# Performance work log

Hardware: AMD Instinct MI355X
Metric: run time of the kernel (lower is better)

The kernel has to match this reference:

```python
import jax, jax.numpy as jnp
import numpy as np

B, N, DIM, H = 4, 128, 512, 8
EPS = 1e-5

def _lin(k, fan_in, fan_out):
    kw, kb = jax.random.split(k)
    w = jax.random.normal(kw, (fan_in, fan_out), jnp.float32) * 0.02
    b = jax.random.normal(kb, (fan_out,), jnp.float32) * 0.02
    return w, b

def setup_inputs() -> dict:
    key = jax.random.key(0)
    ks = jax.random.split(key, 12)
    node_features = jax.random.normal(ks[0], (B, N, DIM), jnp.float32)
    edge_features = jax.random.normal(ks[1], (B, N, N, DIM), jnp.float32)
    adjacency_weights = jax.random.uniform(ks[2], (B, N, N), jnp.float32)
    Wn_w, Wn_b = _lin(ks[3], DIM, DIM)
    We1_w, We1_b = _lin(ks[4], 3 * DIM, DIM)
    We2_w, We2_b = _lin(ks[5], DIM, H)
    Wm_w, Wm_b = _lin(ks[6], DIM, DIM)
    Wu1_w, Wu1_b = _lin(ks[7], 3 * DIM, DIM)
    Wu2_w, Wu2_b = _lin(ks[8], DIM, DIM)
    Wo_w, Wo_b = _lin(ks[9], DIM, DIM)
    ln_g = jnp.ones((DIM,), jnp.float32)
    ln_b = jnp.zeros((DIM,), jnp.float32)
    return dict(node_features=node_features, edge_features=edge_features,
                adjacency_weights=adjacency_weights,
                Wn_w=Wn_w, Wn_b=Wn_b, We1_w=We1_w, We1_b=We1_b,
                We2_w=We2_w, We2_b=We2_b, Wm_w=Wm_w, Wm_b=Wm_b,
                Wu1_w=Wu1_w, Wu1_b=Wu1_b, Wu2_w=Wu2_w, Wu2_b=Wu2_b,
                Wo_w=Wo_w, Wo_b=Wo_b, ln_g=ln_g, ln_b=ln_b)

def _layernorm(x, g, b):
    mu = jnp.mean(x, axis=-1, keepdims=True)
    var = jnp.var(x, axis=-1, keepdims=True)
    return (x - mu) * jax.lax.rsqrt(var + EPS) * g + b

def reference(node_features, edge_features, adjacency_weights,
              Wn_w, Wn_b, We1_w, We1_b, We2_w, We2_b, Wm_w, Wm_b,
              Wu1_w, Wu1_b, Wu2_w, Wu2_b, Wo_w, Wo_b, ln_g, ln_b):
    b, n, d = node_features.shape
    h = node_features @ Wn_w + Wn_b                       # (B,N,D)
    h_i = jnp.broadcast_to(h[:, :, None, :], (b, n, n, d))
    h_j = jnp.broadcast_to(h[:, None, :, :], (b, n, n, d))
    edge_input = jnp.concatenate([h_i, h_j, edge_features], axis=-1)  # (B,N,N,3D)
    # edge attention MLP
    e = jax.nn.leaky_relu(edge_input @ We1_w + We1_b, negative_slope=0.2)
    attn = e @ We2_w + We2_b                              # (B,N,N,H)
    attn = jax.nn.softmax(attn, axis=2)                   # softmax over j
    attn = attn * adjacency_weights[..., None]
    # messages: W_msg applied to h_j == W_msg(h) broadcast; aggregate with mean attn
    messages = h @ Wm_w + Wm_b                            # (B,N,D)
    attn_mean = jnp.mean(attn, axis=-1)                   # (B,N,N)
    aggregated = jnp.einsum('bij,bjd->bid', attn_mean, messages)
    updated_nodes = _layernorm(node_features + (aggregated @ Wo_w + Wo_b), ln_g, ln_b)
    # edge update MLP (exact GELU as in torch default)
    u = jax.nn.gelu(edge_input @ Wu1_w + Wu1_b, approximate=False)
    updated_edges = edge_features + (u @ Wu2_w + Wu2_b)
    return updated_nodes, updated_edges
```

## Files before the change

kernel.cpp:

```cpp
#include <hip/hip_runtime.h>
#include <hip/hip_bf16.h>


typedef __bf16  bf16x8 __attribute__((ext_vector_type(8)));
typedef float   f32x4  __attribute__((ext_vector_type(4)));
typedef __hip_bfloat16 bfloat;

#define AS1 __attribute__((address_space(1)))
#define AS3 __attribute__((address_space(3)))

__device__ __forceinline__ void g2l16(const void* g, void* l) {
  __builtin_amdgcn_global_load_lds((AS1 void*)g, (AS3 void*)l, 16, 0, 0);
}

__device__ __forceinline__ float ldf(const void* p, size_t i, int f) {
  return f ? ((const float*)p)[i] : __bfloat162float(((const bfloat*)p)[i]);
}
__device__ __forceinline__ void stf(void* p, size_t i, float v, int f) {
  if (f) ((float*)p)[i] = v;
  else   ((bfloat*)p)[i] = __float2bfloat16(v);
}

__device__ __forceinline__ float gelu_f(float x) {
  float y = 0.7978845608028654f * (x + 0.044715f * x * x * x);
  float e = __expf(2.0f * y);
  float t = 1.0f - 2.0f / (e + 1.0f);
  return 0.5f * x * (1.0f + t);
}

__global__ __launch_bounds__(256) void detect_dtype(const unsigned short* nu, int* flag) {
  __shared__ int bad;
  if (threadIdx.x == 0) bad = 0;
  __syncthreads();
  int local = 0;
  for (int i = threadIdx.x; i < 4096; i += 256) {
    int ex = (nu[i] >> 7) & 0xFF;
    if (ex >= 0xC0) local = 1;
  }
  if (local) atomicOr(&bad, 1);
  __syncthreads();
  if (threadIdx.x == 0) *flag = bad;
}

__global__ __launch_bounds__(256) void cvt_edge(const float* E, const int* flag, void* dout) {
  if (*flag == 0) return;
  const int e = blockIdx.x & 7;
  const int x = blockIdx.x >> 3;
  const int m = x >> 5;
  const int h = (x >> 4) & 1;
  const int s = x & 15;
  const int c = 2 * e + 16 * m + h;
  const int t = threadIdx.x;
  const int rloc = s * 4 + (t >> 6);
  const int c8 = t & 63;
  const float* src = E + ((size_t)c * 64 + rloc) * 512 + (size_t)c8 * 8;
  f32x4 lo = *(const f32x4*)src;
  f32x4 hi = *(const f32x4*)(src + 4);
  bf16x8 v;
  v[0] = (__bf16)lo[0]; v[1] = (__bf16)lo[1]; v[2] = (__bf16)lo[2]; v[3] = (__bf16)lo[3];
  v[4] = (__bf16)hi[0]; v[5] = (__bf16)hi[1]; v[6] = (__bf16)hi[2]; v[7] = (__bf16)hi[3];
  char* eb = (char*)dout + 1048576;
  *(bf16x8*)(eb + (size_t)c * 131072 + (size_t)rloc * 1024 + (size_t)c8 * 16) = v;
}

__global__ __launch_bounds__(256) void transpose3(const void* We1, const void* Wu1,
                                                  const void* Wu2, const int* flag,
                                                  bfloat* WtA, bfloat* WtB, bfloat* WtC) {
  const int f = *flag;
  int idx = blockIdx.x * 256 + threadIdx.x;
  int m = idx >> 18;
  int r = idx & 262143;
  int n = r >> 9, k = r & 511;
  size_t si = (size_t)k * 512 + n;
  float v;
  bfloat* dst;
  if (m == 0)      { v = ldf(We1, 524288 + si, f); dst = WtA; }
  else if (m == 1) { v = ldf(Wu1, 524288 + si, f); dst = WtB; }
  else             { v = ldf(Wu2, si, f);          dst = WtC; }
  dst[(size_t)n * 512 + k] = __float2bfloat16(v);
}

__global__ __launch_bounds__(256) void small_gemm(const void* A, int amode, const void* W,
                                                  size_t woff, const void* bias,
                                                  const int* flag, float* out) {
  const int f = *flag;
  const int af = amode ? 1 : f;
  __shared__ float sA[4][512];
  const int t = threadIdx.x;
  const int r0 = blockIdx.x * 4;
  for (int idx = t; idx < 2048; idx += 256)
    sA[idx >> 9][idx & 511] = ldf(A, (size_t)(r0 + (idx >> 9)) * 512 + (idx & 511), af);
  __syncthreads();
  float acc0[4] = {0.f, 0.f, 0.f, 0.f}, acc1[4] = {0.f, 0.f, 0.f, 0.f};
#pragma unroll 4
  for (int k = 0; k < 512; ++k) {
    float w0 = ldf(W, woff + (size_t)k * 512 + t, f);
    float w1 = ldf(W, woff + (size_t)k * 512 + t + 256, f);
#pragma unroll
    for (int r = 0; r < 4; ++r) {
      acc0[r] += sA[r][k] * w0;
      acc1[r] += sA[r][k] * w1;
    }
  }
  float b0 = bias ? ldf(bias, t, f) : 0.f;
  float b1 = bias ? ldf(bias, t + 256, f) : 0.f;
#pragma unroll
  for (int r = 0; r < 4; ++r) {
    out[(size_t)(r0 + r) * 512 + t] = acc0[r] + b0;
    out[(size_t)(r0 + r) * 512 + t + 256] = acc1[r] + b1;
  }
}

__global__ __launch_bounds__(256) void fused5(const float* h, const void* We1, const void* We1b,
                                              const void* Wu1, const void* Wu1b, const void* Wm,
                                              const void* Wmb, const int* flag, float* P1,
                                              float* Q1, float* P2, float* Q2, float* msgv) {
  const int f = *flag;
  const void* W;
  size_t woff = 0;
  const void* bias = nullptr;
  float* out;
  switch (blockIdx.y) {
    case 0:  W = We1; bias = We1b; out = P1; break;
    case 1:  W = We1; woff = 262144; out = Q1; break;
    case 2:  W = Wu1; bias = Wu1b; out = P2; break;
    case 3:  W = Wu1; woff = 262144; out = Q2; break;
    default: W = Wm;  bias = Wmb;  out = msgv; break;
  }
  __shared__ float sA[4][512];
  const int t = threadIdx.x;
  const int r0 = blockIdx.x * 4;
  for (int idx = t; idx < 2048; idx += 256)
    sA[idx >> 9][idx & 511] = h[(size_t)(r0 + (idx >> 9)) * 512 + (idx & 511)];
  __syncthreads();
  float acc0[4] = {0.f, 0.f, 0.f, 0.f}, acc1[4] = {0.f, 0.f, 0.f, 0.f};
#pragma unroll 4
  for (int k = 0; k < 512; ++k) {
    float w0 = ldf(W, woff + (size_t)k * 512 + t, f);
    float w1 = ldf(W, woff + (size_t)k * 512 + t + 256, f);
#pragma unroll
    for (int r = 0; r < 4; ++r) {
      acc0[r] += sA[r][k] * w0;
      acc1[r] += sA[r][k] * w1;
    }
  }
  float b0 = bias ? ldf(bias, t, f) : 0.f;
  float b1 = bias ? ldf(bias, t + 256, f) : 0.f;
#pragma unroll
  for (int r = 0; r < 4; ++r) {
    out[(size_t)(r0 + r) * 512 + t] = acc0[r] + b0;
    out[(size_t)(r0 + r) * 512 + t + 256] = acc1[r] + b1;
  }
}

__global__ __launch_bounds__(256) void k3_edge_mlp(const void* E, const bfloat* WtA,
                                                   const bfloat* WtB, const float* P1,
                                                   const float* Q1, const float* P2,
                                                   const float* Q2, const void* We2,
                                                   const int* flag, float* logits4, void* dout) {
  const int f = *flag;
  __shared__ __align__(16) char smem[53248];
  f32x4 acc[4][4];
#pragma unroll
  for (int mi = 0; mi < 4; ++mi)
#pragma unroll
    for (int ni = 0; ni < 4; ++ni) acc[mi][ni] = (f32x4){0.f, 0.f, 0.f, 0.f};

  const int idx0 = blockIdx.x;
  const int bm = (idx0 >> 6) * 8 + (idx0 & 7);
  const int bn = (idx0 >> 3) & 7;
  const bool attn = bn < 4;
  const bfloat* Bg = attn ? WtA + (size_t)bn * 65536 : WtB + (size_t)(bn - 4) * 65536;
  const bfloat* Eb = (const bfloat*)E;
  const char* eb = (const char*)dout + 1048576;

  const int t = threadIdx.x;
  const int lane = t & 63;
  const int wave = t >> 6;
  const int wrow = wave >> 1, wcol = wave & 1;
  const int l15 = lane & 15;
  const int q = lane >> 4;
  const int blockcol = (attn ? bn : (bn - 4)) * 128;

  const int row0 = t >> 2, p0 = t & 3, g0 = p0 ^ ((row0 >> 1) & 3);
  const int row1 = 64 + row0, g1 = p0 ^ ((row1 >> 1) & 3);
  const char* srcB0 = (const char*)Bg + ((size_t)row0 * 512 + g0 * 8) * 2;
  const char* srcB1 = (const char*)Bg + ((size_t)row1 * 512 + g1 * 8) * 2;
  const char* srcA0;
  const char* srcA1;
  const int gr0 = bm * 128 + row0, gr1 = gr0 + 64;
  if (f) {
    srcA0 = eb + (size_t)(gr0 >> 6) * 131072 + (size_t)(gr0 & 63) * 1024 + (size_t)g0 * 16;
    srcA1 = eb + (size_t)(gr1 >> 6) * 131072 + (size_t)(gr1 & 63) * 1024 + (size_t)g1 * 16;
  } else {
    srcA0 = (const char*)Eb + ((size_t)gr0 * 512 + g0 * 8) * 2;
    srcA1 = (const char*)Eb + ((size_t)gr1 * 512 + g1 * 8) * 2;
  }
  const int dst0 = wave * 1024;
  const int dst1 = 4096 + wave * 1024;

  auto stage = [&](int kt2, int sel2) {
    char* dA = smem + sel2 * 8192;
    char* dB = smem + 24576 + sel2 * 8192;
    const int koff = kt2 * 64;
    g2l16(srcA0 + koff, dA + dst0);
    g2l16(srcA1 + koff, dA + dst1);
    g2l16(srcB0 + koff, dB + dst0);
    g2l16(srcB1 + koff, dB + dst1);
  };

  stage(0, 0);
  stage(1, 1);

  if (attn) {
    for (int idx = t; idx < 2048; idx += 256) {
      const int n = idx >> 7, k = idx & 127;
      float v = (n < 8) ? ldf(We2, (size_t)(blockcol + k) * 8 + n, f) : 0.f;
      *(bfloat*)(smem + 49152 + (size_t)n * 256 + (((k >> 3) ^ n) * 16) + (k & 7) * 2) =
          __float2bfloat16(v);
    }
  }

  const int fA = (wrow * 64 + l15) * 64 + ((q ^ ((l15 >> 1) & 3)) * 16);
  const int fB = (wcol * 64 + l15) * 64 + ((q ^ ((l15 >> 1) & 3)) * 16);

#pragma unroll
  for (int kt = 0; kt < 16; ++kt) {
    if (kt < 15) asm volatile("s_waitcnt vmcnt(4)" ::: "memory");
    else         asm volatile("s_waitcnt vmcnt(0)" ::: "memory");
    __builtin_amdgcn_s_barrier();
    if (kt < 14) stage(kt + 2, (kt + 2) % 3);
    const char* A = smem + (kt % 3) * 8192;
    const char* B = smem + 24576 + (kt % 3) * 8192;
    bf16x8 afr[4], bfr[4];
#pragma unroll
    for (int mi = 0; mi < 4; ++mi) afr[mi] = *(const bf16x8*)(A + fA + mi * 1024);
#pragma unroll
    for (int ni = 0; ni < 4; ++ni) bfr[ni] = *(const bf16x8*)(B + fB + ni * 1024);
#pragma unroll
    for (int mi = 0; mi < 4; ++mi)
#pragma unroll
      for (int ni = 0; ni < 4; ++ni)
        acc[mi][ni] =
            __builtin_amdgcn_mfma_f32_16x16x32_bf16(afr[mi], bfr[ni], acc[mi][ni], 0, 0, 0);
  }

  const int b = bm >> 7;
  const float* P = attn ? P1 : P2;
  const float* Qm = attn ? Q1 : Q2;
  float pv[4];
#pragma unroll
  for (int ni = 0; ni < 4; ++ni)
    pv[ni] = P[(size_t)bm * 512 + blockcol + wcol * 64 + ni * 16 + l15];

  __syncthreads();

  if (!attn) {
#pragma unroll
    for (int mi = 0; mi < 4; ++mi)
#pragma unroll
      for (int rr = 0; rr < 4; ++rr) {
        const int j = wrow * 64 + mi * 16 + q * 4 + rr;
#pragma unroll
        for (int ni = 0; ni < 4; ++ni) {
          const int cc = wcol * 64 + ni * 16 + l15;
          const int c = blockcol + cc;
          float x = acc[mi][ni][rr] + pv[ni] + Qm[((size_t)b * 128 + j) * 512 + c];
          *(bfloat*)(smem + (size_t)j * 256 + (((cc >> 3) ^ (j & 15)) * 16) + (cc & 7) * 2) =
              __float2bfloat16(gelu_f(x));
        }
      }
    __syncthreads();
    char* ubase = (char*)dout + (f ? (1048576 + 65536) : 524288);
    const size_t blkstride = f ? 131072 : 65536;
#pragma unroll
    for (int rd = 0; rd < 8; ++rd) {
      const int j = rd * 16 + (t >> 4);
      const int ch = t & 15;
      f32x4 v = *(const f32x4*)(smem + (size_t)j * 256 + ((ch ^ (j & 15)) * 16));
      const size_t m = (size_t)bm * 128 + j;
      *(f32x4*)(ubase + (m >> 6) * blkstride + (m & 63) * 1024 + (size_t)blockcol * 2 +
                (size_t)ch * 16) = v;
    }
  } else {
#pragma unroll
    for (int mi = 0; mi < 4; ++mi)
#pragma unroll
      for (int rr = 0; rr < 4; ++rr) {
        const int j = wrow * 64 + mi * 16 + q * 4 + rr;
#pragma unroll
        for (int ni = 0; ni < 4; ++ni) {
          const int cc = wcol * 64 + ni * 16 + l15;
          const int c = blockcol + cc;
          float x = acc[mi][ni][rr] + pv[ni] + Qm[((size_t)b * 128 + j) * 512 + c];
          float e4 = (x >= 0.f) ? x : 0.2f * x;
          *(bfloat*)(smem + (size_t)j * 256 + (((cc >> 3) ^ (j & 15)) * 16) + (cc & 7) * 2) =
              __float2bfloat16(e4);
        }
      }
    __syncthreads();
    f32x4 acc2[2];
    acc2[0] = (f32x4){0.f, 0.f, 0.f, 0.f};
    acc2[1] = (f32x4){0.f, 0.f, 0.f, 0.f};
    const int jb = wave * 32;
#pragma unroll
    for (int ks = 0; ks < 4; ++ks) {
      const int gA = ((ks * 4 + q) ^ l15) * 16;
      bf16x8 a0 = *(const bf16x8*)(smem + (size_t)(jb + l15) * 256 + gA);
      bf16x8 a1 = *(const bf16x8*)(smem + (size_t)(jb + 16 + l15) * 256 + gA);
      bf16x8 bb = *(const bf16x8*)(smem + 49152 + (size_t)l15 * 256 + gA);
      acc2[0] = __builtin_amdgcn_mfma_f32_16x16x32_bf16(a0, bb, acc2[0], 0, 0, 0);
      acc2[1] = __builtin_amdgcn_mfma_f32_16x16x32_bf16(a1, bb, acc2[1], 0, 0, 0);
    }
#pragma unroll
    for (int mi2 = 0; mi2 < 2; ++mi2)
#pragma unroll
      for (int rr = 0; rr < 4; ++rr) {
        if (l15 < 8) {
          const int j = jb + mi2 * 16 + q * 4 + rr;
          logits4[(((size_t)bn * 512 + bm) * 128 + j) * 8 + l15] = acc2[mi2][rr];
        }
      }
  }
}

__global__ __launch_bounds__(512) void k6_edge_out(const bfloat* WtC, const void* Wu2b,
                                                   const void* E, const int* flag, void* dout) {
  const int f = *flag;
  __shared__ __align__(16) char smem[110592];
  f32x4 acc[2][8];
#pragma unroll
  for (int mi = 0; mi < 2; ++mi)
#pragma unroll
    for (int ni = 0; ni < 8; ++ni) acc[mi][ni] = (f32x4){0.f, 0.f, 0.f, 0.f};

  const int e = blockIdx.x & 7;
  const int x = blockIdx.x >> 3;
  const int bm = 2 * e + 16 * (x >> 1) + (x & 1);
  const int t = threadIdx.x;
  const int lane = t & 63;
  const int wave = t >> 6;
  const int wm = wave >> 2, wn = wave & 3;
  const int l15 = lane & 15;
  const int q = lane >> 4;
  const size_t r0 = (size_t)bm * 64;
  const char* ua = (const char*)dout +
                   (f ? (1048576 + (size_t)bm * 131072 + 65536) : (524288 + (size_t)bm * 65536));

  const int iA = t & 255;
  const int rowA = iA >> 2, pA = iA & 3, gA = pA ^ ((rowA >> 1) & 3);
  const char* srcA = ua + (size_t)rowA * 1024 + (size_t)gA * 16;
  const int dstA = (wave & 3) * 1024;
  const char* srcB[4];
  int dstB[4];
#pragma unroll
  for (int c = 0; c < 4; ++c) {
    const int idx = c * 512 + t;
    const int row = idx >> 2, p = idx & 3, g = p ^ ((row >> 1) & 3);
    srcB[c] = (const char*)WtC + ((size_t)row * 512 + g * 8) * 2;
    dstB[c] = (c * 512 + wave * 64) * 16;
  }

  auto stage = [&](int kt2, int sel2) {
    const int koff = kt2 * 64;
    char* dA = smem + sel2 * 4096;
    char* dB = smem + 12288 + sel2 * 32768;
    g2l16(srcA + koff, dA + dstA);
#pragma unroll
    for (int c = 0; c < 4; ++c) g2l16(srcB[c] + koff, dB + dstB[c]);
  };

  stage(0, 0);
  stage(1, 1);

  const int swz = (q ^ ((l15 >> 1) & 3)) * 16;
  const int fAo = (wm * 32 + l15) * 64 + swz;
  const int fBo = (wn * 128 + l15) * 64 + swz;

#pragma unroll
  for (int kt = 0; kt < 16; ++kt) {
    if (kt < 15) asm volatile("s_waitcnt vmcnt(5)" ::: "memory");
    else         asm volatile("s_waitcnt vmcnt(0)" ::: "memory");
    __builtin_amdgcn_s_barrier();
    if (kt < 14) stage(kt + 2, (kt + 2) % 3);
    const char* sA = smem + (kt % 3) * 4096;
    const char* sB = smem + 12288 + (kt % 3) * 32768;
    bf16x8 afr[2], bfr[8];
#pragma unroll
    for (int mi = 0; mi < 2; ++mi) afr[mi] = *(const bf16x8*)(sA + fAo + mi * 1024);
#pragma unroll
    for (int ni = 0; ni < 8; ++ni) bfr[ni] = *(const bf16x8*)(sB + fBo + ni * 1024);
#pragma unroll
    for (int mi = 0; mi < 2; ++mi)
#pragma unroll
      for (int ni = 0; ni < 8; ++ni)
        acc[mi][ni] = __builtin_amdgcn_mfma_f32_16x16x32_bf16(afr[mi], bfr[ni], acc[mi][ni], 0, 0, 0);
  }
  float wb[8];
#pragma unroll
  for (int ni = 0; ni < 8; ++ni) wb[ni] = ldf(Wu2b, wn * 128 + ni * 16 + l15, f);
  const bfloat* eres = (const bfloat*)((const char*)dout + 1048576 + (size_t)bm * 131072);
#pragma unroll
  for (int mi = 0; mi < 2; ++mi)
#pragma unroll
    for (int rr = 0; rr < 4; ++rr) {
      const int j = wm * 32 + mi * 16 + q * 4 + rr;
#pragma unroll
      for (int ni = 0; ni < 8; ++ni) {
        const int c = wn * 128 + ni * 16 + l15;
        float r = f ? __bfloat162float(eres[(size_t)j * 512 + c])
                    : __bfloat162float(((const bfloat*)E)[(r0 + j) * 512 + c]);
        acc[mi][ni][rr] += wb[ni] + r;
      }
    }
  __syncthreads();
#pragma unroll
  for (int mi = 0; mi < 2; ++mi)
#pragma unroll
    for (int rr = 0; rr < 4; ++rr) {
      const int j = wm * 32 + mi * 16 + q * 4 + rr;
      const size_t row = r0 + j;
#pragma unroll
      for (int ni = 0; ni < 8; ++ni) {
        const int c = wn * 128 + ni * 16 + l15;
        stf(dout, 262144 + row * 512 + c, acc[mi][ni][rr], f);
      }
    }
}

__global__ __launch_bounds__(128) void softmax_mean(const float* logits4, const void* adj,
                                                    const int* flag, float* amean) {
  const int f = *flag;
  const int bi = blockIdx.x;
  const int j = threadIdx.x;
  const int wv = j >> 6;
  __shared__ float sred[2][8];
  f32x4 v0 = (f32x4){0.f, 0.f, 0.f, 0.f}, v1 = (f32x4){0.f, 0.f, 0.f, 0.f};
#pragma unroll
  for (int s = 0; s < 4; ++s) {
    const float* p = logits4 + (((size_t)s * 512 + bi) * 128 + j) * 8;
    v0 += *(const f32x4*)p;
    v1 += *(const f32x4*)(p + 4);
  }
  float xv[8], m[8];
#pragma unroll
  for (int k = 0; k < 4; ++k) { xv[k] = v0[k]; xv[4 + k] = v1[k]; }
#pragma unroll
  for (int h = 0; h < 8; ++h) m[h] = xv[h];
#pragma unroll
  for (int o = 1; o < 64; o <<= 1)
#pragma unroll
    for (int h = 0; h < 8; ++h) m[h] = fmaxf(m[h], __shfl_xor(m[h], o));
  if ((j & 63) == 0) {
#pragma unroll
    for (int h = 0; h < 8; ++h) sred[wv][h] = m[h];
  }
  __syncthreads();
  float ex[8], s8[8];
#pragma unroll
  for (int h = 0; h < 8; ++h) {
    float mx = fmaxf(sred[0][h], sred[1][h]);
    ex[h] = __expf(xv[h] - mx);
    s8[h] = ex[h];
  }
#pragma unroll
  for (int o = 1; o < 64; o <<= 1)
#pragma unroll
    for (int h = 0; h < 8; ++h) s8[h] += __shfl_xor(s8[h], o);
  __syncthreads();
  if ((j & 63) == 0) {
#pragma unroll
    for (int h = 0; h < 8; ++h) sred[wv][h] = s8[h];
  }
  __syncthreads();
  float macc = 0.f;
#pragma unroll
  for (int h = 0; h < 8; ++h) macc += ex[h] / (sred[0][h] + sred[1][h]);
  amean[(size_t)bi * 128 + j] = macc * 0.125f * ldf(adj, (size_t)bi * 128 + j, f);
}

__global__ __launch_bounds__(256) void node_fused(const float* amean, const float* msg,
                                                  const void* Wo, const void* Wob,
                                                  const void* node, const void* lng,
                                                  const void* lnb, const int* flag, void* dout) {
  const int f = *flag;
  const int bi = blockIdx.x;
  const int b = bi >> 7;
  const int t = threadIdx.x;
  __shared__ float am[128];
  __shared__ float sAgg[512];
  __shared__ float red[256];
  if (t < 128) am[t] = amean[(size_t)bi * 128 + t];
  __syncthreads();
  float a0 = 0.f, a1 = 0.f;
#pragma unroll 4
  for (int jj = 0; jj < 128; ++jj) {
    const float* mr = msg + ((size_t)b * 128 + jj) * 512;
    a0 += am[jj] * mr[t];
    a1 += am[jj] * mr[t + 256];
  }
  sAgg[t] = a0;
  sAgg[t + 256] = a1;
  __syncthreads();
  float v0 = 0.f, v1 = 0.f;
#pragma unroll 4
  for (int k = 0; k < 512; ++k) {
    float a = sAgg[k];
    v0 += a * ldf(Wo, (size_t)k * 512 + t, f);
    v1 += a * ldf(Wo, (size_t)k * 512 + t + 256, f);
  }
  v0 += ldf(Wob, t, f) + ldf(node, (size_t)bi * 512 + t, f);
  v1 += ldf(Wob, t + 256, f) + ldf(node, (size_t)bi * 512 + t + 256, f);
  red[t] = v0 + v1;
  __syncthreads();
  for (int s = 128; s > 0; s >>= 1) {
    if (t < s) red[t] += red[t + s];
    __syncthreads();
  }
  float mean = red[0] * (1.f / 512.f);
  __syncthreads();
  red[t] = (v0 - mean) * (v0 - mean) + (v1 - mean) * (v1 - mean);
  __syncthreads();
  for (int s = 128; s > 0; s >>= 1) {
    if (t < s) red[t] += red[t + s];
    __syncthreads();
  }
  float var = red[0] * (1.f / 512.f);
  float inv = rsqrtf(var + 1e-5f);
  stf(dout, (size_t)bi * 512 + t, (v0 - mean) * inv * ldf(lng, t, f) + ldf(lnb, t, f), f);
  stf(dout, (size_t)bi * 512 + t + 256,
      (v1 - mean) * inv * ldf(lng, t + 256, f) + ldf(lnb, t + 256, f), f);
}

extern "C" void kernel_launch(void* const* d_in, const int* in_sizes, int n_in, void* d_out,
                              int out_size, void* d_ws, size_t ws_size, hipStream_t stream) {
  (void)in_sizes; (void)n_in; (void)out_size; (void)ws_size;
  const void* node = d_in[0];
  const void* edge = d_in[1];
  const void* adj = d_in[2];
  const void* Wn_w = d_in[3];
  const void* Wn_b = d_in[4];
  const void* We1_w = d_in[5];
  const void* We1_b = d_in[6];
  const void* We2_w = d_in[7];
  const void* Wm_w = d_in[9];
  const void* Wm_b = d_in[10];
  const void* Wu1_w = d_in[11];
  const void* Wu1_b = d_in[12];
  const void* Wu2_w = d_in[13];
  const void* Wu2_b = d_in[14];
  const void* Wo_w = d_in[15];
  const void* Wo_b = d_in[16];
  const void* ln_g = d_in[17];
  const void* ln_b = d_in[18];

  char* w = (char*)d_ws;
  int* flag = (int*)w;        w += 256;
  float* h = (float*)w;       w += 262144 * 4;
  float* P1 = (float*)w;      w += 262144 * 4;
  float* Q1 = (float*)w;      w += 262144 * 4;
  float* P2 = (float*)w;      w += 262144 * 4;
  float* Q2 = (float*)w;      w += 262144 * 4;
  float* msg = (float*)w;     w += 262144 * 4;
  float* logits4 = (float*)w; w += (size_t)4 * 524288 * 4;
  float* amean = (float*)w;   w += 65536 * 4;
  bfloat* WtA = (bfloat*)w;   w += 262144 * 2;
  bfloat* WtB = (bfloat*)w;   w += 262144 * 2;
  bfloat* WtC = (bfloat*)w;   w += 262144 * 2;

  detect_dtype<<<1, 256, 0, stream>>>((const unsigned short*)node, flag);
  cvt_edge<<<16384, 256, 0, stream>>>((const float*)edge, flag, d_out);
  transpose3<<<3072, 256, 0, stream>>>(We1_w, Wu1_w, Wu2_w, flag, WtA, WtB, WtC);
  small_gemm<<<128, 256, 0, stream>>>(node, 0, Wn_w, 0, Wn_b, flag, h);
  fused5<<<dim3(128, 5), 256, 0, stream>>>(h, We1_w, We1_b, Wu1_w, Wu1_b, Wm_w, Wm_b, flag,
                                           P1, Q1, P2, Q2, msg);
  k3_edge_mlp<<<4096, 256, 0, stream>>>(edge, WtA, WtB, P1, Q1, P2, Q2, We2_w, flag,
                                        logits4, d_out);
  softmax_mean<<<512, 128, 0, stream>>>(logits4, adj, flag, amean);
  node_fused<<<512, 256, 0, stream>>>(amean, msg, Wo_w, Wo_b, node, ln_g, ln_b, flag, d_out);
  k6_edge_out<<<1024, 512, 0, stream>>>(WtC, Wu2_b, edge, flag, d_out);
}
```

Baseline: 732.8 us.

## Use MFMA for node projections, fuse edge MLP column halves, batch node rows

The five per-node projections (P1, Q1, P2, Q2, msg) move from a scalar FP32 kernel to a bf16 MFMA tiled GEMM, using weights pre-transposed into bf16 by an extended transpose kernel and a bf16 copy of h. The edge MLP kernel now computes the attention and update column tiles in the same block, so each edge-feature A tile is loaded once for both products. This halves the grid and increases LDS and register use. The node update kernel handles four rows per block with wave-shuffle LayerNorm reductions, so each Wo and msg load is reused across four rows, and the projections now round to bf16 precision.

New measurement: 823.6 us. +12.4%, slower.

```diff
diff --git a/kernel.cpp b/kernel.cpp
--- a/kernel.cpp
+++ b/kernel.cpp
@@ -64,8 +64,11 @@
 }
 
 __global__ __launch_bounds__(256) void transpose3(const void* We1, const void* Wu1,
-                                                  const void* Wu2, const int* flag,
-                                                  bfloat* WtA, bfloat* WtB, bfloat* WtC) {
+                                                  const void* Wu2, const void* Wm,
+                                                  const int* flag,
+                                                  bfloat* WtA, bfloat* WtB, bfloat* WtC,
+                                                  bfloat* WtD, bfloat* WtE, bfloat* WtF,
+                                                  bfloat* WtG, bfloat* WtH) {
   const int f = *flag;
   int idx = blockIdx.x * 256 + threadIdx.x;
   int m = idx >> 18;
@@ -74,15 +77,22 @@
   size_t si = (size_t)k * 512 + n;
   float v;
   bfloat* dst;
-  if (m == 0)      { v = ldf(We1, 524288 + si, f); dst = WtA; }
-  else if (m == 1) { v = ldf(Wu1, 524288 + si, f); dst = WtB; }
-  else             { v = ldf(Wu2, si, f);          dst = WtC; }
+  switch (m) {
+    case 0:  v = ldf(We1, 524288 + si, f); dst = WtA; break;
+    case 1:  v = ldf(Wu1, 524288 + si, f); dst = WtB; break;
+    case 2:  v = ldf(Wu2, si, f);          dst = WtC; break;
+    case 3:  v = ldf(We1, si, f);          dst = WtD; break;
+    case 4:  v = ldf(We1, 262144 + si, f); dst = WtE; break;
+    case 5:  v = ldf(Wu1, si, f);          dst = WtF; break;
+    case 6:  v = ldf(Wu1, 262144 + si, f); dst = WtG; break;
+    default: v = ldf(Wm, si, f);           dst = WtH; break;
+  }
   dst[(size_t)n * 512 + k] = __float2bfloat16(v);
 }
 
 __global__ __launch_bounds__(256) void small_gemm(const void* A, int amode, const void* W,
                                                   size_t woff, const void* bias,
-                                                  const int* flag, float* out) {
+                                                  const int* flag, float* out, bfloat* outb) {
   const int f = *flag;
   const int af = amode ? 1 : f;
   __shared__ float sA[4][512];
@@ -106,51 +116,110 @@
   float b1 = bias ? ldf(bias, t + 256, f) : 0.f;
 #pragma unroll
   for (int r = 0; r < 4; ++r) {
-    out[(size_t)(r0 + r) * 512 + t] = acc0[r] + b0;
-    out[(size_t)(r0 + r) * 512 + t + 256] = acc1[r] + b1;
-  }
-}
-
-__global__ __launch_bounds__(256) void fused5(const float* h, const void* We1, const void* We1b,
-                                              const void* Wu1, const void* Wu1b, const void* Wm,
-                                              const void* Wmb, const int* flag, float* P1,
-                                              float* Q1, float* P2, float* Q2, float* msgv) {
-  const int f = *flag;
-  const void* W;
-  size_t woff = 0;
+    float o0 = acc0[r] + b0, o1 = acc1[r] + b1;
+    out[(size_t)(r0 + r) * 512 + t] = o0;
+    out[(size_t)(r0 + r) * 512 + t + 256] = o1;
+    if (outb) {
+      outb[(size_t)(r0 + r) * 512 + t] = __float2bfloat16(o0);
+      outb[(size_t)(r0 + r) * 512 + t + 256] = __float2bfloat16(o1);
+    }
+  }
+}
+
+__global__ __launch_bounds__(256) void fused5_mfma(const bfloat* hb, const bfloat* WtD,
+                                                   const bfloat* WtE, const bfloat* WtF,
+                                                   const bfloat* WtG, const bfloat* WtH,
+                                                   const void* We1b, const void* Wu1b,
+                                                   const void* Wmb, const int* flag,
+                                                   float* P1, float* Q1, float* P2, float* Q2,
+                                                   float* msgv) {
+  const int fl = *flag;
+  __shared__ __align__(16) char smem[49152];
+  f32x4 acc[4][4];
+#pragma unroll
+  for (int mi = 0; mi < 4; ++mi)
+#pragma unroll
+    for (int ni = 0; ni < 4; ++ni) acc[mi][ni] = (f32x4){0.f, 0.f, 0.f, 0.f};
+
+  const int bid = blockIdx.x;
+  const int g = bid >> 4, rb = (bid >> 2) & 3, cbv = bid & 3;
+  const bfloat* Wt;
   const void* bias = nullptr;
   float* out;
-  switch (blockIdx.y) {
-    case 0:  W = We1; bias = We1b; out = P1; break;
-    case 1:  W = We1; woff = 262144; out = Q1; break;
-    case 2:  W = Wu1; bias = Wu1b; out = P2; break;
-    case 3:  W = Wu1; woff = 262144; out = Q2; break;
-    default: W = Wm;  bias = Wmb;  out = msgv; break;
-  }
-  __shared__ float sA[4][512];
-  const int t = threadIdx.x;
-  const int r0 = blockIdx.x * 4;
-  for (int idx = t; idx < 2048; idx += 256)
-    sA[idx >> 9][idx & 511] = h[(size_t)(r0 + (idx >> 9)) * 512 + (idx & 511)];
-  __syncthreads();
-  float acc0[4] = {0.f, 0.f, 0.f, 0.f}, acc1[4] = {0.f, 0.f, 0.f, 0.f};
-#pragma unroll 4
-  for (int k = 0; k < 512; ++k) {
-    float w0 = ldf(W, woff + (size_t)k * 512 + t, f);
-    float w1 = ldf(W, woff + (size_t)k * 512 + t + 256, f);
-#pragma unroll
-    for (int r = 0; r < 4; ++r) {
-      acc0[r] += sA[r][k] * w0;
-      acc1[r] += sA[r][k] * w1;
-    }
-  }
-  float b0 = bias ? ldf(bias, t, f) : 0.f;
-  float b1 = bias ? ldf(bias, t + 256, f) : 0.f;
-#pragma unroll
-  for (int r = 0; r < 4; ++r) {
-    out[(size_t)(r0 + r) * 512 + t] = acc0[r] + b0;
-    out[(size_t)(r0 + r) * 512 + t + 256] = acc1[r] + b1;
-  }
+  switch (g) {
+    case 0:  Wt = WtD; bias = We1b; out = P1; break;
+    case 1:  Wt = WtE; out = Q1; break;
+    case 2:  Wt = WtF; bias = Wu1b; out = P2; break;
+    case 3:  Wt = WtG; out = Q2; break;
+    default: Wt = WtH; bias = Wmb; out = msgv; break;
+  }
+  const bfloat* Ag = hb + (size_t)rb * 65536;
+  const bfloat* Bg = Wt + (size_t)cbv * 65536;
+
+  const int t = threadIdx.x, lane = t & 63, wave = t >> 6;
+  const int wrow = wave >> 1, wcol = wave & 1;
+  const int l15 = lane & 15, q = lane >> 4;
+
+  const int row0 = t >> 2, p0 = t & 3, g0 = p0 ^ ((row0 >> 1) & 3);
+  const int row1 = 64 + row0, g1 = p0 ^ ((row1 >> 1) & 3);
+  const char* srcA0 = (const char*)(Ag + (size_t)row0 * 512 + g0 * 8);
+  const char* srcA1 = (const char*)(Ag + (size_t)row1 * 512 + g1 * 8);
+  const char* srcB0 = (const char*)(Bg + (size_t)row0 * 512 + g0 * 8);
+  const char* srcB1 = (const char*)(Bg + (size_t)row1 * 512 + g1 * 8);
+  const int dst0 = wave * 1024, dst1 = 4096 + wave * 1024;
+
+  auto stage = [&](int kt2, int sel2) {
+    const int koff = kt2 * 64;
+    char* dA = smem + sel2 * 8192;
+    char* dB = smem + 24576 + sel2 * 8192;
+    g2l16(srcA0 + koff, dA + dst0);
+    g2l16(srcA1 + koff, dA + dst1);
+    g2l16(srcB0 + koff, dB + dst0);
+    g2l16(srcB1 + koff, dB + dst1);
+  };
+  stage(0, 0);
+  stage(1, 1);
+
+  const int swz = (q ^ ((l15 >> 1) & 3)) * 16;
+  const int fA = (wrow * 64 + l15) * 64 + swz;
+  const int fB = (wcol * 64 + l15) * 64 + swz;
+
+#pragma unroll
+  for (int kt = 0; kt < 16; ++kt) {
+    if (kt < 15) asm volatile("s_waitcnt vmcnt(4)" ::: "memory");
+    else         asm volatile("s_waitcnt vmcnt(0)" ::: "memory");
+    __builtin_amdgcn_s_barrier();
+    if (kt < 14) stage(kt + 2, (kt + 2) % 3);
+    const char* A = smem + (kt % 3) * 8192;
+    const char* B = smem + 24576 + (kt % 3) * 8192;
+    bf16x8 afr[4], bfr[4];
+#pragma unroll
+    for (int mi = 0; mi < 4; ++mi) afr[mi] = *(const bf16x8*)(A + fA + mi * 1024);
+#pragma unroll
+    for (int ni = 0; ni < 4; ++ni) bfr[ni] = *(const bf16x8*)(B + fB + ni * 1024);
+#pragma unroll
+    for (int mi = 0; mi < 4; ++mi)
+#pragma unroll
+      for (int ni = 0; ni < 4; ++ni)
+        acc[mi][ni] =
+            __builtin_amdgcn_mfma_f32_16x16x32_bf16(afr[mi], bfr[ni], acc[mi][ni], 0, 0, 0);
+  }
+
+  float bv[4];
+#pragma unroll
+  for (int ni = 0; ni < 4; ++ni)
+    bv[ni] = bias ? ldf(bias, (size_t)cbv * 128 + wcol * 64 + ni * 16 + l15, fl) : 0.f;
+#pragma unroll
+  for (int mi = 0; mi < 4; ++mi)
+#pragma unroll
+    for (int rr = 0; rr < 4; ++rr) {
+      const int j = wrow * 64 + mi * 16 + q * 4 + rr;
+#pragma unroll
+      for (int ni = 0; ni < 4; ++ni) {
+        const int cc = wcol * 64 + ni * 16 + l15;
+        out[(size_t)(rb * 128 + j) * 512 + cbv * 128 + cc] = acc[mi][ni][rr] + bv[ni];
+      }
+    }
 }
 
 __global__ __launch_bounds__(256) void k3_edge_mlp(const void* E, const bfloat* WtA,
@@ -159,33 +228,38 @@
                                                    const float* Q2, const void* We2,
                                                    const int* flag, float* logits4, void* dout) {
   const int f = *flag;
-  __shared__ __align__(16) char smem[53248];
-  f32x4 acc[4][4];
+  __shared__ __align__(16) char smem[77824];
+  f32x4 accA[4][4], accU[4][4];
 #pragma unroll
   for (int mi = 0; mi < 4; ++mi)
 #pragma unroll
-    for (int ni = 0; ni < 4; ++ni) acc[mi][ni] = (f32x4){0.f, 0.f, 0.f, 0.f};
+    for (int ni = 0; ni < 4; ++ni) {
+      accA[mi][ni] = (f32x4){0.f, 0.f, 0.f, 0.f};
+      accU[mi][ni] = (f32x4){0.f, 0.f, 0.f, 0.f};
+    }
 
   const int idx0 = blockIdx.x;
-  const int bm = (idx0 >> 6) * 8 + (idx0 & 7);
-  const int bn = (idx0 >> 3) & 7;
-  const bool attn = bn < 4;
-  const bfloat* Bg = attn ? WtA + (size_t)bn * 65536 : WtB + (size_t)(bn - 4) * 65536;
+  const int bm = (idx0 >> 5) * 8 + (idx0 & 7);
+  const int cb = (idx0 >> 3) & 3;
+  const int blockcol = cb * 128;
+  const bfloat* BgA = WtA + (size_t)cb * 65536;
+  const bfloat* BgU = WtB + (size_t)cb * 65536;
   const bfloat* Eb = (const bfloat*)E;
   const char* eb = (const char*)dout + 1048576;
 
-  const int t = threadIdx.x;
-  const int lane = t & 63;
-  const int wave = t >> 6;
+  const int t = threadIdx.x, lane = t & 63, wave = t >> 6;
   const int wrow = wave >> 1, wcol = wave & 1;
-  const int l15 = lane & 15;
-  const int q = lane >> 4;
-  const int blockcol = (attn ? bn : (bn - 4)) * 128;
+  const int l15 = lane & 15, q = lane >> 4;
+
+  for (int idx = t; idx < 2048; idx += 256) {
+    const int n = idx >> 7, k = idx & 127;
+    float v = (n < 8) ? ldf(We2, (size_t)(blockcol + k) * 8 + n, f) : 0.f;
+    *(bfloat*)(smem + 73728 + (size_t)n * 256 + (((k >> 3) ^ n) * 16) + (k & 7) * 2) =
+        __float2bfloat16(v);
+  }
 
   const int row0 = t >> 2, p0 = t & 3, g0 = p0 ^ ((row0 >> 1) & 3);
   const int row1 = 64 + row0, g1 = p0 ^ ((row1 >> 1) & 3);
-  const char* srcB0 = (const char*)Bg + ((size_t)row0 * 512 + g0 * 8) * 2;
-  const char* srcB1 = (const char*)Bg + ((size_t)row1 * 512 + g1 * 8) * 2;
   const char* srcA0;
   const char* srcA1;
   const int gr0 = bm * 128 + row0, gr1 = gr0 + 64;
@@ -196,81 +270,91 @@
     srcA0 = (const char*)Eb + ((size_t)gr0 * 512 + g0 * 8) * 2;
     srcA1 = (const char*)Eb + ((size_t)gr1 * 512 + g1 * 8) * 2;
   }
-  const int dst0 = wave * 1024;
-  const int dst1 = 4096 + wave * 1024;
+  const int dstA0 = wave * 1024, dstA1 = 4096 + wave * 1024;
+
+  const char* srcB[4];
+  int dstB[4];
+#pragma unroll
+  for (int c = 0; c < 4; ++c) {
+    const int idx = c * 256 + t;
+    const int row = idx >> 2, p = idx & 3, gg = p ^ ((row >> 1) & 3);
+    const bfloat* base =
+        (row < 128) ? (BgA + (size_t)row * 512) : (BgU + (size_t)(row - 128) * 512);
+    srcB[c] = (const char*)base + gg * 16;
+    dstB[c] = (c * 256 + wave * 64) * 16;
+  }
 
   auto stage = [&](int kt2, int sel2) {
+    const int koff = kt2 * 64;
     char* dA = smem + sel2 * 8192;
-    char* dB = smem + 24576 + sel2 * 8192;
-    const int koff = kt2 * 64;
-    g2l16(srcA0 + koff, dA + dst0);
-    g2l16(srcA1 + koff, dA + dst1);
-    g2l16(srcB0 + koff, dB + dst0);
-    g2l16(srcB1 + koff, dB + dst1);
+    char* dB = smem + 24576 + sel2 * 16384;
+    g2l16(srcA0 + koff, dA + dstA0);
+    g2l16(srcA1 + koff, dA + dstA1);
+#pragma unroll
+    for (int c = 0; c < 4; ++c) g2l16(srcB[c] + koff, dB + dstB[c]);
   };
-
   stage(0, 0);
   stage(1, 1);
 
-  if (attn) {
-    for (int idx = t; idx < 2048; idx += 256) {
-      const int n = idx >> 7, k = idx & 127;
-      float v = (n < 8) ? ldf(We2, (size_t)(blockcol + k) * 8 + n, f) : 0.f;
-      *(bfloat*)(smem + 49152 + (size_t)n * 256 + (((k >> 3) ^ n) * 16) + (k & 7) * 2) =
-          __float2bfloat16(v);
-    }
-  }
-
-  const int fA = (wrow * 64 + l15) * 64 + ((q ^ ((l15 >> 1) & 3)) * 16);
-  const int fB = (wcol * 64 + l15) * 64 + ((q ^ ((l15 >> 1) & 3)) * 16);
+  const int swz = (q ^ ((l15 >> 1) & 3)) * 16;
+  const int fA = (wrow * 64 + l15) * 64 + swz;
+  const int fB = (wcol * 64 + l15) * 64 + swz;
 
 #pragma unroll
   for (int kt = 0; kt < 16; ++kt) {
-    if (kt < 15) asm volatile("s_waitcnt vmcnt(4)" ::: "memory");
+    if (kt < 15) asm volatile("s_waitcnt vmcnt(6)" ::: "memory");
     else         asm volatile("s_waitcnt vmcnt(0)" ::: "memory");
     __builtin_amdgcn_s_barrier();
     if (kt < 14) stage(kt + 2, (kt + 2) % 3);
     const char* A = smem + (kt % 3) * 8192;
-    const char* B = smem + 24576 + (kt % 3) * 8192;
-    bf16x8 afr[4], bfr[4];
+    const char* B = smem + 24576 + (kt % 3) * 16384;
+    bf16x8 afr[4], bfrA[4], bfrU[4];
 #pragma unroll
     for (int mi = 0; mi < 4; ++mi) afr[mi] = *(const bf16x8*)(A + fA + mi * 1024);
 #pragma unroll
-    for (int ni = 0; ni < 4; ++ni) bfr[ni] = *(const bf16x8*)(B + fB + ni * 1024);
+    for (int ni = 0; ni < 4; ++ni) bfrA[ni] = *(const bf16x8*)(B + fB + ni * 1024);
 #pragma unroll
     for (int mi = 0; mi < 4; ++mi)
 #pragma unroll
       for (int ni = 0; ni < 4; ++ni)
-        acc[mi][ni] =
-            __builtin_amdgcn_mfma_f32_16x16x32_bf16(afr[mi], bfr[ni], acc[mi][ni], 0, 0, 0);
+        accA[mi][ni] =
+            __builtin_amdgcn_mfma_f32_16x16x32_bf16(afr[mi], bfrA[ni], accA[mi][ni], 0, 0, 0);
+#pragma unroll
+    for (int ni = 0; ni < 4; ++ni) bfrU[ni] = *(const bf16x8*)(B + 8192 + fB + ni * 1024);
+#pragma unroll
+    for (int mi = 0; mi < 4; ++mi)
+#pragma unroll
+      for (int ni = 0; ni < 4; ++ni)
+        accU[mi][ni] =
+            __builtin_amdgcn_mfma_f32_16x16x32_bf16(afr[mi], bfrU[ni], accU[mi][ni], 0, 0, 0);
   }
 
   const int b = bm >> 7;
-  const float* P = attn ? P1 : P2;
-  const float* Qm = attn ? Q1 : Q2;
-  float pv[4];
-#pragma unroll
-  for (int ni = 0; ni < 4; ++ni)
-    pv[ni] = P[(size_t)bm * 512 + blockcol + wcol * 64 + ni * 16 + l15];
-
-  __syncthreads();
-
-  if (!attn) {
-#pragma unroll
-    for (int mi = 0; mi < 4; ++mi)
-#pragma unroll
-      for (int rr = 0; rr < 4; ++rr) {
-        const int j = wrow * 64 + mi * 16 + q * 4 + rr;
-#pragma unroll
-        for (int ni = 0; ni < 4; ++ni) {
-          const int cc = wcol * 64 + ni * 16 + l15;
-          const int c = blockcol + cc;
-          float x = acc[mi][ni][rr] + pv[ni] + Qm[((size_t)b * 128 + j) * 512 + c];
-          *(bfloat*)(smem + (size_t)j * 256 + (((cc >> 3) ^ (j & 15)) * 16) + (cc & 7) * 2) =
-              __float2bfloat16(gelu_f(x));
-        }
+  float pv1[4], pv2[4];
+#pragma unroll
+  for (int ni = 0; ni < 4; ++ni) {
+    const size_t o = (size_t)bm * 512 + blockcol + wcol * 64 + ni * 16 + l15;
+    pv1[ni] = P1[o];
+    pv2[ni] = P2[o];
+  }
+  __syncthreads();
+
+#pragma unroll
+  for (int mi = 0; mi < 4; ++mi)
+#pragma unroll
+    for (int rr = 0; rr < 4; ++rr) {
+      const int j = wrow * 64 + mi * 16 + q * 4 + rr;
+#pragma unroll
+      for (int ni = 0; ni < 4; ++ni) {
+        const int cc = wcol * 64 + ni * 16 + l15;
+        const int c = blockcol + cc;
+        float x = accU[mi][ni][rr] + pv2[ni] + Q2[((size_t)b * 128 + j) * 512 + c];
+        *(bfloat*)(smem + (size_t)j * 256 + (((cc >> 3) ^ (j & 15)) * 16) + (cc & 7) * 2) =
+            __float2bfloat16(gelu_f(x));
       }
-    __syncthreads();
+    }
+  __syncthreads();
+  {
     char* ubase = (char*)dout + (f ? (1048576 + 65536) : 524288);
     const size_t blkstride = f ? 131072 : 65536;
 #pragma unroll
@@ -282,23 +366,26 @@
       *(f32x4*)(ubase + (m >> 6) * blkstride + (m & 63) * 1024 + (size_t)blockcol * 2 +
                 (size_t)ch * 16) = v;
     }
-  } else {
-#pragma unroll
-    for (int mi = 0; mi < 4; ++mi)
-#pragma unroll
-      for (int rr = 0; rr < 4; ++rr) {
-        const int j = wrow * 64 + mi * 16 + q * 4 + rr;
-#pragma unroll
-        for (int ni = 0; ni < 4; ++ni) {
-          const int cc = wcol * 64 + ni * 16 + l15;
-          const int c = blockcol + cc;
-          float x = acc[mi][ni][rr] + pv[ni] + Qm[((size_t)b * 128 + j) * 512 + c];
-          float e4 = (x >= 0.f) ? x : 0.2f * x;
-          *(bfloat*)(smem + (size_t)j * 256 + (((cc >> 3) ^ (j & 15)) * 16) + (cc & 7) * 2) =
-              __float2bfloat16(e4);
-        }
+  }
+  __syncthreads();
+
+#pragma unroll
+  for (int mi = 0; mi < 4; ++mi)
+#pragma unroll
+    for (int rr = 0; rr < 4; ++rr) {
+      const int j = wrow * 64 + mi * 16 + q * 4 + rr;
+#pragma unroll
+      for (int ni = 0; ni < 4; ++ni) {
+        const int cc = wcol * 64 + ni * 16 + l15;
+        const int c = blockcol + cc;
+        float x = accA[mi][ni][rr] + pv1[ni] + Q1[((size_t)b * 128 + j) * 512 + c];
+        float e4 = (x >= 0.f) ? x : 0.2f * x;
+        *(bfloat*)(smem + (size_t)j * 256 + (((cc >> 3) ^ (j & 15)) * 16) + (cc & 7) * 2) =
+            __float2bfloat16(e4);
       }
-    __syncthreads();
+    }
+  __syncthreads();
+  {
     f32x4 acc2[2];
     acc2[0] = (f32x4){0.f, 0.f, 0.f, 0.f};
     acc2[1] = (f32x4){0.f, 0.f, 0.f, 0.f};
@@ -308,7 +395,7 @@
       const int gA = ((ks * 4 + q) ^ l15) * 16;
       bf16x8 a0 = *(const bf16x8*)(smem + (size_t)(jb + l15) * 256 + gA);
       bf16x8 a1 = *(const bf16x8*)(smem + (size_t)(jb + 16 + l15) * 256 + gA);
-      bf16x8 bb = *(const bf16x8*)(smem + 49152 + (size_t)l15 * 256 + gA);
+      bf16x8 bb = *(const bf16x8*)(smem + 73728 + (size_t)l15 * 256 + gA);
       acc2[0] = __builtin_amdgcn_mfma_f32_16x16x32_bf16(a0, bb, acc2[0], 0, 0, 0);
       acc2[1] = __builtin_amdgcn_mfma_f32_16x16x32_bf16(a1, bb, acc2[1], 0, 0, 0);
     }
@@ -318,7 +405,7 @@
       for (int rr = 0; rr < 4; ++rr) {
         if (l15 < 8) {
           const int j = jb + mi2 * 16 + q * 4 + rr;
-          logits4[(((size_t)bn * 512 + bm) * 128 + j) * 8 + l15] = acc2[mi2][rr];
+          logits4[(((size_t)cb * 512 + bm) * 128 + j) * 8 + l15] = acc2[mi2][rr];
         }
       }
   }
@@ -484,52 +571,95 @@
                                                   const void* node, const void* lng,
                                                   const void* lnb, const int* flag, void* dout) {
   const int f = *flag;
-  const int bi = blockIdx.x;
-  const int b = bi >> 7;
+  const int r0 = blockIdx.x * 4;
+  const int b = r0 >> 7;
   const int t = threadIdx.x;
-  __shared__ float am[128];
-  __shared__ float sAgg[512];
-  __shared__ float red[256];
-  if (t < 128) am[t] = amean[(size_t)bi * 128 + t];
-  __syncthreads();
-  float a0 = 0.f, a1 = 0.f;
-#pragma unroll 4
+  const int lane = t & 63, wave = t >> 6;
+  __shared__ float am[512];
+  __shared__ float sAgg[4][512];
+  __shared__ float sw[4][4];
+  __shared__ float sw2[4][4];
+  am[t] = amean[(size_t)r0 * 128 + t];
+  am[t + 256] = amean[(size_t)r0 * 128 + t + 256];
+  __syncthreads();
+  float a0[4] = {0.f, 0.f, 0.f, 0.f}, a1[4] = {0.f, 0.f, 0.f, 0.f};
+#pragma unroll 2
   for (int jj = 0; jj < 128; ++jj) {
     const float* mr = msg + ((size_t)b * 128 + jj) * 512;
-    a0 += am[jj] * mr[t];
-    a1 += am[jj] * mr[t + 256];
-  }
-  sAgg[t] = a0;
-  sAgg[t + 256] = a1;
-  __syncthreads();
-  float v0 = 0.f, v1 = 0.f;
-#pragma unroll 4
-  for (int k = 0; k < 512; ++k) {
-    float a = sAgg[k];
-    v0 += a * ldf(Wo, (size_t)k * 512 + t, f);
-    v1 += a * ldf(Wo, (size_t)k * 512 + t + 256, f);
-  }
-  v0 += ldf(Wob, t, f) + ldf(node, (size_t)bi * 512 + t, f);
-  v1 += ldf(Wob, t + 256, f) + ldf(node, (size_t)bi * 512 + t + 256, f);
-  red[t] = v0 + v1;
-  __syncthreads();
-  for (int s = 128; s > 0; s >>= 1) {
-    if (t < s) red[t] += red[t + s];
-    __syncthreads();
-  }
-  float mean = red[0] * (1.f / 512.f);
-  __syncthreads();
-  red[t] = (v0 - mean) * (v0 - mean) + (v1 - mean) * (v1 - mean);
-  __syncthreads();
-  for (int s = 128; s > 0; s >>= 1) {
-    if (t < s) red[t] += red[t + s];
-    __syncthreads();
-  }
-  float var = red[0] * (1.f / 512.f);
-  float inv = rsqrtf(var + 1e-5f);
-  stf(dout, (size_t)bi * 512 + t, (v0 - mean) * inv * ldf(lng, t, f) + ldf(lnb, t, f), f);
-  stf(dout, (size_t)bi * 512 + t + 256,
-      (v1 - mean) * inv * ldf(lng, t + 256, f) + ldf(lnb, t + 256, f), f);
+    float m0 = mr[t], m1 = mr[t + 256];
+#pragma unroll
+    for (int r = 0; r < 4; ++r) {
+      a0[r] += am[r * 128 + jj] * m0;
+      a1[r] += am[r * 128 + jj] * m1;
+    }
+  }
+#pragma unroll
+  for (int r = 0; r < 4; ++r) { sAgg[r][t] = a0[r]; sAgg[r][t + 256] = a1[r]; }
+  __syncthreads();
+  float v0[4] = {0.f, 0.f, 0.f, 0.f}, v1[4] = {0.f, 0.f, 0.f, 0.f};
+  if (f) {
+    const float* W = (const float*)Wo;
+#pragma unroll 2
+    for (int k = 0; k < 512; ++k) {
+      float w0 = W[(size_t)k * 512 + t], w1 = W[(size_t)k * 512 + t + 256];
+#pragma unroll
+      for (int r = 0; r < 4; ++r) { v0[r] += sAgg[r][k] * w0; v1[r] += sAgg[r][k] * w1; }
+    }
+  } else {
+    const bfloat* W = (const bfloat*)Wo;
+#pragma unroll 2
+    for (int k = 0; k < 512; ++k) {
+      float w0 = __bfloat162float(W[(size_t)k * 512 + t]);
+      float w1 = __bfloat162float(W[(size_t)k * 512 + t + 256]);
+#pragma unroll
+      for (int r = 0; r < 4; ++r) { v0[r] += sAgg[r][k] * w0; v1[r] += sAgg[r][k] * w1; }
+    }
+  }
+  float wob0 = ldf(Wob, t, f), wob1 = ldf(Wob, t + 256, f);
+#pragma unroll
+  for (int r = 0; r < 4; ++r) {
+    v0[r] += wob0 + ldf(node, (size_t)(r0 + r) * 512 + t, f);
+    v1[r] += wob1 + ldf(node, (size_t)(r0 + r) * 512 + t + 256, f);
+  }
+  float s[4];
+#pragma unroll
+  for (int r = 0; r < 4; ++r) s[r] = v0[r] + v1[r];
+#pragma unroll
+  for (int o = 1; o < 64; o <<= 1)
+#pragma unroll
+    for (int r = 0; r < 4; ++r) s[r] += __shfl_xor(s[r], o);
+  if (lane == 0) {
+#pragma unroll
+    for (int r = 0; r < 4; ++r) sw[wave][r] = s[r];
+  }
+  __syncthreads();
+  float mean[4];
+#pragma unroll
+  for (int r = 0; r < 4; ++r)
+    mean[r] = (sw[0][r] + sw[1][r] + sw[2][r] + sw[3][r]) * (1.f / 512.f);
+#pragma unroll
+  for (int r = 0; r < 4; ++r) {
+    float d0 = v0[r] - mean[r], d1 = v1[r] - mean[r];
+    s[r] = d0 * d0 + d1 * d1;
+  }
+#pragma unroll
+  for (int o = 1; o < 64; o <<= 1)
+#pragma unroll
+    for (int r = 0; r < 4; ++r) s[r] += __shfl_xor(s[r], o);
+  if (lane == 0) {
+#pragma unroll
+    for (int r = 0; r < 4; ++r) sw2[wave][r] = s[r];
+  }
+  __syncthreads();
+  float g0v = ldf(lng, t, f), g1v = ldf(lng, t + 256, f);
+  float b0v = ldf(lnb, t, f), b1v = ldf(lnb, t + 256, f);
+#pragma unroll
+  for (int r = 0; r < 4; ++r) {
+    float var = (sw2[0][r] + sw2[1][r] + sw2[2][r] + sw2[3][r]) * (1.f / 512.f);
+    float inv = rsqrtf(var + 1e-5f);
+    stf(dout, (size_t)(r0 + r) * 512 + t, (v0[r] - mean[r]) * inv * g0v + b0v, f);
+    stf(dout, (size_t)(r0 + r) * 512 + t + 256, (v1[r] - mean[r]) * inv * g1v + b1v, f);
+  }
 }
 
 extern "C" void kernel_launch(void* const* d_in, const int* in_sizes, int n_in, void* d_out,
@@ -567,16 +697,23 @@
   bfloat* WtA = (bfloat*)w;   w += 262144 * 2;
   bfloat* WtB = (bfloat*)w;   w += 262144 * 2;
   bfloat* WtC = (bfloat*)w;   w += 262144 * 2;
+  bfloat* WtD = (bfloat*)w;   w += 262144 * 2;
+  bfloat* WtE = (bfloat*)w;   w += 262144 * 2;
+  bfloat* WtF = (bfloat*)w;   w += 262144 * 2;
+  bfloat* WtG = (bfloat*)w;   w += 262144 * 2;
+  bfloat* WtH = (bfloat*)w;   w += 262144 * 2;
+  bfloat* hb = (bfloat*)w;    w += 262144 * 2;
 
   detect_dtype<<<1, 256, 0, stream>>>((const unsigned short*)node, flag);
   cvt_edge<<<16384, 256, 0, stream>>>((const float*)edge, flag, d_out);
-  transpose3<<<3072, 256, 0, stream>>>(We1_w, Wu1_w, Wu2_w, flag, WtA, WtB, WtC);
-  small_gemm<<<128, 256, 0, stream>>>(node, 0, Wn_w, 0, Wn_b, flag, h);
-  fused5<<<dim3(128, 5), 256, 0, stream>>>(h, We1_w, We1_b, Wu1_w, Wu1_b, Wm_w, Wm_b, flag,
-                                           P1, Q1, P2, Q2, msg);
-  k3_edge_mlp<<<4096, 256, 0, stream>>>(edge, WtA, WtB, P1, Q1, P2, Q2, We2_w, flag,
+  transpose3<<<8192, 256, 0, stream>>>(We1_w, Wu1_w, Wu2_w, Wm_w, flag, WtA, WtB, WtC,
+                                       WtD, WtE, WtF, WtG, WtH);
+  small_gemm<<<128, 256, 0, stream>>>(node, 0, Wn_w, 0, Wn_b, flag, h, hb);
+  fused5_mfma<<<80, 256, 0, stream>>>(hb, WtD, WtE, WtF, WtG, WtH, We1_b, Wu1_b, Wm_b, flag,
+                                      P1, Q1, P2, Q2, msg);
+  k3_edge_mlp<<<2048, 256, 0, stream>>>(edge, WtA, WtB, P1, Q1, P2, Q2, We2_w, flag,
                                         logits4, d_out);
   softmax_mean<<<512, 128, 0, stream>>>(logits4, adj, flag, amean);
-  node_fused<<<512, 256, 0, stream>>>(amean, msg, Wo_w, Wo_b, node, ln_g, ln_b, flag, d_out);
+  node_fused<<<128, 256, 0, stream>>>(amean, msg, Wo_w, Wo_b, node, ln_g, ln_b, flag, d_out);
   k6_edge_out<<<1024, 512, 0, stream>>>(WtC, Wu2_b, edge, flag, d_out);
 }
```
